# Performance work log

Hardware: AMD Instinct MI355X
Metric: run time of the kernel (lower is better)

The kernel has to match this reference:

```python
import jax, jax.numpy as jnp
import numpy as np

EPS = 1e-8
ALPHA = 0.3
PATTERN_W = 0.1


def setup_inputs() -> dict:
    key = jax.random.key(0)
    ks = jax.random.split(key, 6)
    H, W, D, Hid = 1024, 1024, 32, 64
    return {
        "grid_states": jax.random.normal(ks[0], (H, W, D), dtype=jnp.float32),
        "potentials": jax.random.uniform(ks[1], (H, W), dtype=jnp.float32),
        "W1": jax.random.normal(ks[2], (D + 1, Hid), dtype=jnp.float32) * 0.1,
        "b1": jax.random.normal(ks[3], (Hid,), dtype=jnp.float32) * 0.1,
        "W2": jax.random.normal(ks[4], (Hid, D), dtype=jnp.float32) * 0.1,
        "b2": jax.random.normal(ks[5], (D,), dtype=jnp.float32) * 0.1,
    }


def reference(grid_states, potentials, W1, b1, W2, b2):
    # self_similarity: A^3 normalized to unit length, rescaled by ||A||
    cube = grid_states * grid_states * grid_states                     # [H,W,D]
    cube_norm = jnp.linalg.norm(cube, axis=-1, keepdims=True)          # [H,W,1]
    cell_norm = jnp.linalg.norm(grid_states, axis=-1, keepdims=True)   # [H,W,1]
    self_pattern = cube / (cube_norm + EPS) * cell_norm                # [H,W,D]

    cell_with_pattern = grid_states + PATTERN_W * self_pattern         # [H,W,D]

    # transform_net on [cell_with_pattern ; potential]
    x = jnp.concatenate([cell_with_pattern, potentials[..., None]], axis=-1)  # [H,W,D+1]
    h = jax.nn.relu(jnp.einsum("hwc,cf->hwf", x, W1) + b1)             # [H,W,Hid]
    transformed = jnp.einsum("hwf,fd->hwd", h, W2) + b2                # [H,W,D]

    # new_state = transform + alpha * cell  (neighbor influence path only
    # affects role_value, which forward() discards)
    return transformed + ALPHA * grid_states
```

## Files before the change

### kernel.cpp

```cpp
#include <hip/hip_runtime.h>

#define DIM   32
#define HID   64
#define TILES 8
#define HPAD  72

typedef __attribute__((ext_vector_type(8))) short bf16x8;
typedef __attribute__((ext_vector_type(4))) float f32x4;

__device__ __forceinline__ short f2bf(float f) {
    union { float f; unsigned u; } v; v.f = f;
    unsigned r = (v.u + 0x7FFFu + ((v.u >> 16) & 1u)) >> 16;
    return (short)r;
}

__global__ __launch_bounds__(256) void behavior_mfma(
    const float* __restrict__ g_in,
    const float* __restrict__ pot,
    const float* __restrict__ W1,
    const float* __restrict__ b1,
    const float* __restrict__ W2,
    const float* __restrict__ b2,
    float* __restrict__ out)
{
    __shared__ __align__(16) short sH[4 * 16 * HPAD];

    const int tid  = threadIdx.x;
    const int lane = tid & 63;
    const int quad = lane >> 4;
    const int mrow = lane & 15;
    const int wave = tid >> 6;
    short* hbase = &sH[wave * 16 * HPAD];

    bf16x8 w1f[4];
    float  w1p[4], b1v[4];
    #pragma unroll
    for (int nb = 0; nb < 4; ++nb) {
        #pragma unroll
        for (int j = 0; j < 8; ++j)
            w1f[nb][j] = f2bf(W1[(quad * 8 + j) * HID + nb * 16 + mrow]);
        w1p[nb] = W1[32 * HID + nb * 16 + mrow];
        b1v[nb] = b1[nb * 16 + mrow];
    }
    bf16x8 w2f[2][2];
    #pragma unroll
    for (int kc = 0; kc < 2; ++kc)
        #pragma unroll
        for (int nc = 0; nc < 2; ++nc)
            #pragma unroll
            for (int j = 0; j < 8; ++j)
                w2f[kc][nc][j] = f2bf(W2[(kc * 32 + quad * 8 + j) * DIM + nc * 16 + mrow]);
    float b2v[2];
    #pragma unroll
    for (int nc = 0; nc < 2; ++nc) b2v[nc] = b2[nc * 16 + mrow];

    bf16x8 idf[2];
    #pragma unroll
    for (int nc = 0; nc < 2; ++nc)
        #pragma unroll
        for (int j = 0; j < 8; ++j)
            idf[nc][j] = (quad * 8 + j == nc * 16 + mrow) ? (short)0x3F80 : (short)0;

    const long wave_id = (long)blockIdx.x * 4 + wave;
    const long cell0   = wave_id * (TILES * 16);

    float4 cga, cgb, cpv;
    {
        const float* gp = g_in + (cell0 + mrow) * DIM + quad * 8;
        cga = ((const float4*)gp)[0];
        cgb = ((const float4*)gp)[1];
        cpv = *(const float4*)(pot + cell0 + quad * 4);
    }

    #pragma unroll
    for (int t = 0; t < TILES; ++t) {
        float4 nga, ngb, npv;
        if (t + 1 < TILES) {
            const long cb = cell0 + (long)(t + 1) * 16;
            const float* gp = g_in + (cb + mrow) * DIM + quad * 8;
            nga = ((const float4*)gp)[0];
            ngb = ((const float4*)gp)[1];
            npv = *(const float4*)(pot + cb + quad * 4);
        }

        const long cb = cell0 + (long)t * 16;
        float gv[8] = {cga.x, cga.y, cga.z, cga.w, cgb.x, cgb.y, cgb.z, cgb.w};
        float pvr[4] = {cpv.x, cpv.y, cpv.z, cpv.w};

        float cube[8];
        float tp = 0.f, sp = 0.f;
        #pragma unroll
        for (int j = 0; j < 8; ++j) {
            float gc = gv[j];
            float g2 = gc * gc;
            float g3 = g2 * gc;
            tp += g2;
            sp = fmaf(g3, g3, sp);
            cube[j] = g3;
        }
        tp += __shfl_xor(tp, 16, 64); tp += __shfl_xor(tp, 32, 64);
        sp += __shfl_xor(sp, 16, 64); sp += __shfl_xor(sp, 32, 64);
        const float scale = 0.1f * sqrtf(tp) / (sqrtf(sp) + 1e-8f);

        bf16x8 xf, gf;
        #pragma unroll
        for (int j = 0; j < 8; ++j) {
            xf[j] = f2bf(fmaf(scale, cube[j], gv[j]));
            gf[j] = f2bf(0.3f * gv[j]);
        }

        #pragma unroll
        for (int nb = 0; nb < 4; ++nb) {
            f32x4 c1;
            #pragma unroll
            for (int r = 0; r < 4; ++r) c1[r] = fmaf(pvr[r], w1p[nb], b1v[nb]);
            c1 = __builtin_amdgcn_mfma_f32_16x16x32_bf16(xf, w1f[nb], c1, 0, 0, 0);
            #pragma unroll
            for (int r = 0; r < 4; ++r)
                hbase[(quad * 4 + r) * HPAD + nb * 16 + mrow] = f2bf(fmaxf(c1[r], 0.f));
        }

        bf16x8 hf0 = *(const bf16x8*)&hbase[mrow * HPAD +  0 + quad * 8];
        bf16x8 hf1 = *(const bf16x8*)&hbase[mrow * HPAD + 32 + quad * 8];

        #pragma unroll
        for (int nc = 0; nc < 2; ++nc) {
            f32x4 c2 = {b2v[nc], b2v[nc], b2v[nc], b2v[nc]};
            c2 = __builtin_amdgcn_mfma_f32_16x16x32_bf16(gf, idf[nc],    c2, 0, 0, 0);
            c2 = __builtin_amdgcn_mfma_f32_16x16x32_bf16(hf0, w2f[0][nc], c2, 0, 0, 0);
            c2 = __builtin_amdgcn_mfma_f32_16x16x32_bf16(hf1, w2f[1][nc], c2, 0, 0, 0);
            #pragma unroll
            for (int r = 0; r < 4; ++r)
                out[(cb + quad * 4 + r) * DIM + nc * 16 + mrow] = c2[r];
        }

        cga = nga; cgb = ngb; cpv = npv;
    }
}

extern "C" void kernel_launch(void* const* d_in, const int* in_sizes, int n_in,
                              void* d_out, int out_size, void* d_ws, size_t ws_size,
                              hipStream_t stream) {
    const float* g_in = (const float*)d_in[0];
    const float* pot  = (const float*)d_in[1];
    const float* W1   = (const float*)d_in[2];
    const float* b1   = (const float*)d_in[3];
    const float* W2   = (const float*)d_in[4];
    const float* b2   = (const float*)d_in[5];
    float* out = (float*)d_out;

    const int n_cells = in_sizes[1];
    const int cells_per_block = 4 * TILES * 16;
    const int blocks = (n_cells + cells_per_block - 1) / cells_per_block;

    behavior_mfma<<<blocks, 256, 0, stream>>>(g_in, pot, W1, b1, W2, b2, out);
}
```

Baseline: 255.1 us.

## Software-pipeline GEMM1 and GEMM2 across tiles with double-buffered LDS

Restructures the per-wave tile loop into a software pipeline. Each iteration computes the first GEMM for tile t into one of two LDS buffers while running the second GEMM and the store for tile t-1 from the other buffer. The aim is to overlap LDS write-to-read latency and MFMA dependency chains with independent work. It doubles the per-wave LDS footprint and raises register pressure, since the hidden-layer fragments and gf for two tiles are live at once. Wave-local LDS with no barrier relies on the same wave's ordering, as before.

```diff
diff --git a/kernel.cpp b/kernel.cpp
--- a/kernel.cpp
+++ b/kernel.cpp
@@ -4,6 +4,7 @@
 #define HID   64
 #define TILES 8
 #define HPAD  72
+#define HBUF  (16 * HPAD)
 
 typedef __attribute__((ext_vector_type(8))) short bf16x8;
 typedef __attribute__((ext_vector_type(4))) float f32x4;
@@ -23,14 +24,14 @@
     const float* __restrict__ b2,
     float* __restrict__ out)
 {
-    __shared__ __align__(16) short sH[4 * 16 * HPAD];
+    __shared__ __align__(16) short sH[4 * 2 * HBUF];
 
     const int tid  = threadIdx.x;
     const int lane = tid & 63;
     const int quad = lane >> 4;
     const int mrow = lane & 15;
     const int wave = tid >> 6;
-    short* hbase = &sH[wave * 16 * HPAD];
+    short* hb = &sH[wave * 2 * HBUF];
 
     bf16x8 w1f[4];
     float  w1p[4], b1v[4];
@@ -61,32 +62,18 @@
         for (int j = 0; j < 8; ++j)
             idf[nc][j] = (quad * 8 + j == nc * 16 + mrow) ? (short)0x3F80 : (short)0;
 
-    const long wave_id = (long)blockIdx.x * 4 + wave;
-    const long cell0   = wave_id * (TILES * 16);
+    const long cell0 = ((long)blockIdx.x * 4 + wave) * (TILES * 16);
 
-    float4 cga, cgb, cpv;
-    {
-        const float* gp = g_in + (cell0 + mrow) * DIM + quad * 8;
-        cga = ((const float4*)gp)[0];
-        cgb = ((const float4*)gp)[1];
-        cpv = *(const float4*)(pot + cell0 + quad * 4);
-    }
+    auto loadTile = [&](long cb, float4& a, float4& b, float4& p) {
+        const float* gp = g_in + (cb + mrow) * DIM + quad * 8;
+        a = ((const float4*)gp)[0];
+        b = ((const float4*)gp)[1];
+        p = *(const float4*)(pot + cb + quad * 4);
+    };
 
-    #pragma unroll
-    for (int t = 0; t < TILES; ++t) {
-        float4 nga, ngb, npv;
-        if (t + 1 < TILES) {
-            const long cb = cell0 + (long)(t + 1) * 16;
-            const float* gp = g_in + (cb + mrow) * DIM + quad * 8;
-            nga = ((const float4*)gp)[0];
-            ngb = ((const float4*)gp)[1];
-            npv = *(const float4*)(pot + cb + quad * 4);
-        }
-
-        const long cb = cell0 + (long)t * 16;
-        float gv[8] = {cga.x, cga.y, cga.z, cga.w, cgb.x, cgb.y, cgb.z, cgb.w};
-        float pvr[4] = {cpv.x, cpv.y, cpv.z, cpv.w};
-
+    auto stageA = [&](const float4& a, const float4& b, const float4& p,
+                      short* buf, bf16x8& gf_out) {
+        float gv[8] = {a.x, a.y, a.z, a.w, b.x, b.y, b.z, b.w};
         float cube[8];
         float tp = 0.f, sp = 0.f;
         #pragma unroll
@@ -102,13 +89,13 @@
         sp += __shfl_xor(sp, 16, 64); sp += __shfl_xor(sp, 32, 64);
         const float scale = 0.1f * sqrtf(tp) / (sqrtf(sp) + 1e-8f);
 
-        bf16x8 xf, gf;
+        bf16x8 xf;
         #pragma unroll
         for (int j = 0; j < 8; ++j) {
-            xf[j] = f2bf(fmaf(scale, cube[j], gv[j]));
-            gf[j] = f2bf(0.3f * gv[j]);
+            xf[j]     = f2bf(fmaf(scale, cube[j], gv[j]));
+            gf_out[j] = f2bf(0.3f * gv[j]);
         }
-
+        const float pvr[4] = {p.x, p.y, p.z, p.w};
         #pragma unroll
         for (int nb = 0; nb < 4; ++nb) {
             f32x4 c1;
@@ -117,24 +104,51 @@
             c1 = __builtin_amdgcn_mfma_f32_16x16x32_bf16(xf, w1f[nb], c1, 0, 0, 0);
             #pragma unroll
             for (int r = 0; r < 4; ++r)
-                hbase[(quad * 4 + r) * HPAD + nb * 16 + mrow] = f2bf(fmaxf(c1[r], 0.f));
+                buf[(quad * 4 + r) * HPAD + nb * 16 + mrow] = f2bf(fmaxf(c1[r], 0.f));
         }
+    };
 
-        bf16x8 hf0 = *(const bf16x8*)&hbase[mrow * HPAD +  0 + quad * 8];
-        bf16x8 hf1 = *(const bf16x8*)&hbase[mrow * HPAD + 32 + quad * 8];
-
+    auto gemm2 = [&](const bf16x8& hf0, const bf16x8& hf1, const bf16x8& gfv, long cb) {
         #pragma unroll
         for (int nc = 0; nc < 2; ++nc) {
             f32x4 c2 = {b2v[nc], b2v[nc], b2v[nc], b2v[nc]};
-            c2 = __builtin_amdgcn_mfma_f32_16x16x32_bf16(gf, idf[nc],    c2, 0, 0, 0);
+            c2 = __builtin_amdgcn_mfma_f32_16x16x32_bf16(gfv, idf[nc],    c2, 0, 0, 0);
             c2 = __builtin_amdgcn_mfma_f32_16x16x32_bf16(hf0, w2f[0][nc], c2, 0, 0, 0);
             c2 = __builtin_amdgcn_mfma_f32_16x16x32_bf16(hf1, w2f[1][nc], c2, 0, 0, 0);
             #pragma unroll
             for (int r = 0; r < 4; ++r)
                 out[(cb + quad * 4 + r) * DIM + nc * 16 + mrow] = c2[r];
         }
+    };
+
+    float4 cga, cgb, cpv, nga, ngb, npv;
+    bf16x8 gfP, gfC;
+
+    loadTile(cell0, cga, cgb, cpv);
+    loadTile(cell0 + 16, nga, ngb, npv);
+    stageA(cga, cgb, cpv, hb, gfP);
+
+    #pragma unroll 2
+    for (int t = 1; t < TILES; ++t) {
+        short* rbuf = hb + ((t - 1) & 1) * HBUF;
+        bf16x8 hf0 = *(const bf16x8*)&rbuf[mrow * HPAD +  0 + quad * 8];
+        bf16x8 hf1 = *(const bf16x8*)&rbuf[mrow * HPAD + 32 + quad * 8];
 
         cga = nga; cgb = ngb; cpv = npv;
+        if (t + 1 < TILES)
+            loadTile(cell0 + (long)(t + 1) * 16, nga, ngb, npv);
+
+        stageA(cga, cgb, cpv, hb + (t & 1) * HBUF, gfC);
+
+        gemm2(hf0, hf1, gfP, cell0 + (long)(t - 1) * 16);
+        gfP = gfC;
+    }
+
+    {
+        short* rbuf = hb + ((TILES - 1) & 1) * HBUF;
+        bf16x8 hf0 = *(const bf16x8*)&rbuf[mrow * HPAD +  0 + quad * 8];
+        bf16x8 hf1 = *(const bf16x8*)&rbuf[mrow * HPAD + 32 + quad * 8];
+        gemm2(hf0, hf1, gfP, cell0 + (long)(TILES - 1) * 16);
     }
 }
 
```

Result: no change. 252.1 us (-1.2%).
